# Kernel tuning notes

Measured on AMD Instinct MI355X. Metric: run time of the kernel, lower is better.

## Reference

```python
import jax, jax.numpy as jnp
import numpy as np
from jax import lax

B, C, H, W = 64, 384, 28, 28
E, K, R = 3, 2, 8          # num_experts, top_k, lora rank
HID = 4 * C                # ConvNeXt MLP hidden
EPS = 1e-6
SCALING = 8.0 / 8.0        # alpha / r


def setup_inputs() -> dict:
    key = jax.random.key(0)
    ks = jax.random.split(key, 18)
    N = B * H * W
    f32 = jnp.float32
    inp = {
        "x": jax.random.normal(ks[0], (B, C, H, W), f32),
        "conv_w": jax.random.normal(ks[1], (C, 1, 7, 7), f32) * 0.05,
        "conv_b": jax.random.normal(ks[2], (C,), f32) * 0.02,
        "norm_g": 1.0 + jax.random.normal(ks[3], (C,), f32) * 0.02,
        "norm_b": jax.random.normal(ks[4], (C,), f32) * 0.02,
        "dom_g": jax.random.normal(ks[5], (E, C), f32) * 0.02,
        "dom_b": jax.random.normal(ks[6], (E, C), f32) * 0.02,
        "fc1_w": jax.random.normal(ks[7], (C, HID), f32) * (C ** -0.5),
        "fc1_b": jax.random.normal(ks[8], (HID,), f32) * 0.02,
        "fc2_w": jax.random.normal(ks[9], (HID, C), f32) * (HID ** -0.5),
        "fc2_b": jax.random.normal(ks[10], (C,), f32) * 0.02,
        "w_down": jax.random.normal(ks[11], (E, C, R), f32) * (C ** -0.5),
        "w_up": jax.random.normal(ks[12], (E, R, C), f32) * 0.02,
        "gamma": jax.random.normal(ks[13], (C,), f32) * 0.1,
        "routing_weights": jax.nn.softmax(jax.random.normal(ks[14], (B, E), f32), axis=-1),
        "topk_probs": jax.nn.softmax(jax.random.normal(ks[15], (N, K), f32), axis=-1),
        "topk_indices": jax.random.randint(ks[16], (N, K), 0, E),
    }
    return inp


def _forward(x, conv_w, conv_b, norm_g, norm_b, dom_g, dom_b,
             fc1_w, fc1_b, fc2_w, fc2_b, w_down, w_up, gamma,
             routing_weights, topk_probs, topk_indices):
    shortcut = x
    # depthwise 7x7 conv, NCHW, SAME padding
    y = lax.conv_general_dilated(
        x, conv_w, window_strides=(1, 1), padding=((3, 3), (3, 3)),
        feature_group_count=C,
        dimension_numbers=("NCHW", "OIHW", "NCHW"))
    y = y + conv_b[None, :, None, None]
    y = jnp.transpose(y, (0, 2, 3, 1))  # [B, H, W, C] channels-last path

    # ParallelMoELayerNorm: orig LN + sum_i w_i * LN_i(x). All LNs share eps,
    # so normalize once and fuse affine params per-sample.
    mu = jnp.mean(y, axis=-1, keepdims=True)
    var = jnp.mean(jnp.square(y - mu), axis=-1, keepdims=True)
    xhat = (y - mu) * lax.rsqrt(var + EPS)
    g_eff = norm_g[None, :] + routing_weights @ dom_g   # [B, C]
    b_eff = norm_b[None, :] + routing_weights @ dom_b   # [B, C]
    y = xhat * g_eff[:, None, None, :] + b_eff[:, None, None, :]

    # base ConvNeXt MLP (exact GELU, as torch nn.GELU)
    h = jax.nn.gelu(jnp.einsum("bhwc,cf->bhwf", y, fc1_w) + fc1_b,
                    approximate=False)
    orig_out = jnp.einsum("bhwf,fc->bhwc", h, fc2_w) + fc2_b

    # MoE LoRA: dense per-expert rank-8 compute, combined with top-k weights.
    # Equivalent math to the gather/matmul/scatter-add loop in the source.
    y_flat = y.reshape(-1, C)                                   # [N, C]
    down = jnp.einsum("nc,ecr->enr", y_flat, w_down)            # [E, N, R]
    up = jnp.einsum("enr,erc->enc", jax.nn.gelu(down, approximate=False), w_up)
    # combine weights: comb[n, e] = sum_k topk_probs[n, k] * (topk_indices[n,k]==e)
    comb = jnp.sum(jax.nn.one_hot(topk_indices, E, dtype=y.dtype)
                   * topk_probs[..., None], axis=1)             # [N, E]
    moe_out = jnp.einsum("enc,ne->nc", up * SCALING, comb)
    y = orig_out + moe_out.reshape(B, H, W, C)

    y = jnp.transpose(y, (0, 3, 1, 2))  # back to NCHW
    y = gamma[None, :, None, None] * y  # layer scale; drop_path = identity (eval)
    return y + shortcut


def reference(x, conv_w, conv_b, norm_g, norm_b, dom_g, dom_b,
              fc1_w, fc1_b, fc2_w, fc2_b, w_down, w_up, gamma,
              routing_weights, topk_probs, topk_indices):
    return _forward(x, conv_w, conv_b, norm_g, norm_b, dom_g, dom_b,
                    fc1_w, fc1_b, fc2_w, fc2_b, w_down, w_up, gamma,
                    routing_weights, topk_probs, topk_indices)
```

## Files before the change

### kernel.cpp

```cpp
#include <hip/hip_runtime.h>
#include <hip/hip_bf16.h>
#include <cstdint>
#include <cstddef>

constexpr int cB   = 64;
constexpr int cC   = 384;
constexpr int cH   = 28;
constexpr int cW   = 28;
constexpr int cHID = 1536;
constexpr int cNTOK = cB * cH * cW;
constexpr int cKP   = cHID + 64;
constexpr int cCH   = 2;
constexpr int cMR   = cNTOK / cCH;

typedef __attribute__((ext_vector_type(8))) short bf16x8;
typedef __attribute__((ext_vector_type(4))) float f32x4;

__device__ __forceinline__ float gelu_f(float x) {
  float u = 1.5957691216057308f * x * (1.0f + 0.044715f * x * x);
  float e = __expf(-u);
  return x / (1.0f + e);
}

__device__ __forceinline__ float bf16_to_f(unsigned short s) {
  return __uint_as_float(((unsigned)s) << 16);
}
__device__ __forceinline__ unsigned short f_to_bf16(float v) {
  __hip_bfloat16 hb = __float2bfloat16(v);
  return *reinterpret_cast<unsigned short*>(&hb);
}

__device__ __forceinline__ void gload_lds16(const void* g, void* l) {
  __builtin_amdgcn_global_load_lds(
      (const __attribute__((address_space(1))) unsigned int*)g,
      (__attribute__((address_space(3))) unsigned int*)l, 16, 0, 0);
}

__device__ __forceinline__ int xcd_remap(int b, int nwg) {
  int qn = nwg >> 3, rm = nwg & 7;
  int xcd = b & 7, off = b >> 3;
  return (xcd < rm) ? xcd * (qn + 1) + off
                    : rm * (qn + 1) + (xcd - rm) * qn + off;
}

__global__ __launch_bounds__(256) void prep_eff(
    const float* __restrict__ ng, const float* __restrict__ nb,
    const float* __restrict__ dg, const float* __restrict__ db,
    const float* __restrict__ rw, float* __restrict__ geff, float* __restrict__ beff) {
  int i = blockIdx.x * 256 + threadIdx.x;
  if (i >= cB * cC) return;
  int b = i / cC, c = i - b * cC;
  float g = ng[c], bb = nb[c];
#pragma unroll
  for (int e = 0; e < 3; ++e) {
    float r = rw[b * 3 + e];
    g += r * dg[e * cC + c];
    bb += r * db[e * cC + c];
  }
  geff[i] = g;
  beff[i] = bb;
}

__global__ __launch_bounds__(256) void transpose_bf16(
    const float* __restrict__ w, __hip_bfloat16* __restrict__ wt, int R0, int C0) {
  __shared__ float t[64][65];
  int c0 = blockIdx.x * 64, r0 = blockIdx.y * 64;
  for (int i = threadIdx.x; i < 64 * 64; i += 256) {
    int r = i >> 6, c = i & 63;
    t[r][c] = w[(size_t)(r0 + r) * C0 + c0 + c];
  }
  __syncthreads();
  for (int i = threadIdx.x; i < 64 * 64; i += 256) {
    int c = i >> 6, r = i & 63;
    wt[(size_t)(c0 + c) * R0 + r0 + r] = __float2bfloat16(t[r][c]);
  }
}

__global__ __launch_bounds__(256) void build_fc2t(
    const float* __restrict__ fc2w, const float* __restrict__ wu,
    __hip_bfloat16* __restrict__ fc2t) {
  int i = blockIdx.x * 256 + threadIdx.x;
  if (i >= cC * cKP) return;
  int c = i / cKP, k = i - c * cKP;
  float v = 0.f;
  if (k < cHID) v = fc2w[(size_t)k * cC + c];
  else {
    int j = k - cHID;
    if (j < 24) v = wu[(size_t)(j >> 3) * 8 * cC + (size_t)(j & 7) * cC + c];
  }
  fc2t[i] = __float2bfloat16(v);
}

__global__ __launch_bounds__(256) void build_wdt(
    const float* __restrict__ wd, __hip_bfloat16* __restrict__ wdt) {
  int i = blockIdx.x * 256 + threadIdx.x;
  if (i >= 32 * cC) return;
  int j = i / cC, c = i - j * cC;
  float v = 0.f;
  if (j < 24) v = wd[(size_t)(j >> 3) * cC * 8 + (size_t)c * 8 + (j & 7)];
  wdt[i] = __float2bfloat16(v);
}

constexpr int cPL = 4;
__global__ __launch_bounds__(128) void conv_dw(
    const float* __restrict__ x, const float* __restrict__ cw,
    const float* __restrict__ cb, __hip_bfloat16* __restrict__ out) {
  int pb = blockIdx.x * cPL;
  int c0 = pb % cC;
  __shared__ __align__(16) float tile[cPL][34][38];
  __shared__ float wsm[cPL][49];
  const int tid = threadIdx.x;

  float2 z2 = {0.f, 0.f};
  for (int i = tid; i < cPL * 34 * 38 / 2; i += 128)
    ((float2*)tile)[i] = z2;
  __syncthreads();

  for (int i = tid; i < cPL * 196; i += 128) {
    int p = i / 196, q = i - p * 196;
    int r = q / 7, cl = (q - r * 7) * 4;
    float4 v = *(const float4*)&x[(size_t)(pb + p) * 784 + r * 28 + cl];
    float* dst = &tile[p][r + 3][cl + 4];
    *(float2*)dst = make_float2(v.x, v.y);
    *(float2*)(dst + 2) = make_float2(v.z, v.w);
  }
  for (int i = tid; i < cPL * 49; i += 128) {
    int p = i / 49, k = i - p * 49;
    wsm[p][k] = cw[(size_t)(c0 + p) * 49 + k];
  }
  __syncthreads();

  if (tid < cPL * 28) {
    int p = tid / 28, r = tid - p * 28;
    float acc[28];
    float cbv = cb[c0 + p];
#pragma unroll
    for (int w = 0; w < 28; ++w) acc[w] = cbv;
    for (int dh = 0; dh < 7; ++dh) {
      float rowv[36];
      const float* rp = &tile[p][r + dh][0];
#pragma unroll
      for (int k = 0; k < 18; ++k)
        ((float2*)rowv)[k] = *(const float2*)(rp + k * 2);
      float w7[7];
#pragma unroll
      for (int dw = 0; dw < 7; ++dw) w7[dw] = wsm[p][dh * 7 + dw];
#pragma unroll
      for (int w = 0; w < 28; ++w)
#pragma unroll
        for (int dw = 0; dw < 7; ++dw)
          acc[w] += rowv[w + dw + 1] * w7[dw];
    }
    unsigned short* op = (unsigned short*)out + (size_t)(pb + p) * 784 + r * 28;
#pragma unroll
    for (int k = 0; k < 7; ++k) {
      ushort4 s;
      s.x = f_to_bf16(acc[k * 4 + 0]);
      s.y = f_to_bf16(acc[k * 4 + 1]);
      s.z = f_to_bf16(acc[k * 4 + 2]);
      s.w = f_to_bf16(acc[k * 4 + 3]);
      *(ushort4*)&op[k * 4] = s;
    }
  }
}

__global__ __launch_bounds__(256) void ln_affine(
    const __hip_bfloat16* __restrict__ convout, const float* __restrict__ geff,
    const float* __restrict__ beff, __hip_bfloat16* __restrict__ y) {
  int bh = blockIdx.x;
  int b = bh / cH;
  int hrow = bh - b * cH;
  __shared__ float t[cC * 29];
  const unsigned short* src =
      (const unsigned short*)convout + (size_t)b * cC * (cH * cW) + (size_t)hrow * cW;
  for (int i = threadIdx.x; i < cC * 7; i += 256) {
    int c = i / 7, wq = (i - c * 7) * 4;
    ushort4 v = *(const ushort4*)&src[(size_t)c * (cH * cW) + wq];
    t[c * 29 + wq + 0] = bf16_to_f(v.x);
    t[c * 29 + wq + 1] = bf16_to_f(v.y);
    t[c * 29 + wq + 2] = bf16_to_f(v.z);
    t[c * 29 + wq + 3] = bf16_to_f(v.w);
  }
  __syncthreads();
  int wave = threadIdx.x >> 6, lane = threadIdx.x & 63;
  const float* gp = geff + (size_t)b * cC;
  const float* bp = beff + (size_t)b * cC;
  for (int w = wave; w < cW; w += 4) {
    float v[6], s = 0.f, s2 = 0.f;
#pragma unroll
    for (int j = 0; j < 6; ++j) {
      v[j] = t[(lane + 64 * j) * 29 + w];
      s += v[j];
      s2 += v[j] * v[j];
    }
#pragma unroll
    for (int d = 32; d; d >>= 1) {
      s += __shfl_xor(s, d);
      s2 += __shfl_xor(s2, d);
    }
    float mu = s * (1.0f / cC);
    float var = s2 * (1.0f / cC) - mu * mu;
    float rstd = rsqrtf(var + 1e-6f);
    size_t n = (size_t)bh * cW + w;
#pragma unroll
    for (int j = 0; j < 6; ++j) {
      int c = lane + 64 * j;
      float val = (v[j] - mu) * rstd * gp[c] + bp[c];
      y[n * cC + c] = __float2bfloat16(val);
    }
  }
}

template <int DO_GELU>
__global__ __launch_bounds__(512) void gemm8(
    const __hip_bfloat16* __restrict__ A, int lda,
    const __hip_bfloat16* __restrict__ Bt,
    const float* __restrict__ bias,
    __hip_bfloat16* __restrict__ Cb, int ldc,
    int M, int N, int K, int NT_N) {
  __shared__ __align__(16) __hip_bfloat16 As[3][256 * 64];
  __shared__ __align__(16) __hip_bfloat16 Bs[3][128 * 64];

  const int bid = xcd_remap(blockIdx.x, gridDim.x);
  const int gsz = 8 * NT_N;
  const int g = bid / gsz;
  const int q = bid - g * gsz;
  const int mi = g * 8 + q / NT_N;
  const int ni = q - (q / NT_N) * NT_N;
  const int m0 = mi * 256, n0 = ni * 128;

  const int tid = threadIdx.x;
  const int lane = tid & 63;
  const int wid = tid >> 6;
  const int wm = wid >> 1;
  const int wn = wid & 1;
  const int l15 = lane & 15, l7 = lane & 7, lq = lane >> 4;

  const __hip_bfloat16* srcA[4];
  const __hip_bfloat16* srcB[2];
  int dstA[4], dstB[2];
#pragma unroll
  for (int a = 0; a < 4; ++a) {
    int gu = a * 512 + tid;
    int row = gu >> 3, pu = gu & 7;
    int u = pu ^ (row & 7);
    srcA[a] = &A[(size_t)(m0 + row) * lda + u * 8];
    dstA[a] = gu * 16;
  }
#pragma unroll
  for (int b = 0; b < 2; ++b) {
    int gu = b * 512 + tid;
    int row = gu >> 3, pu = gu & 7;
    int u = pu ^ (row & 7);
    srcB[b] = &Bt[(size_t)(n0 + row) * K + u * 8];
    dstB[b] = gu * 16;
  }

#define STAGE_A(BUF)                                         \
  do {                                                       \
    _Pragma("unroll") for (int a = 0; a < 4; ++a) {          \
      gload_lds16(srcA[a], (char*)As[BUF] + dstA[a]);        \
      srcA[a] += 64;                                         \
    }                                                        \
  } while (0)
#define STAGE_B(BUF)                                         \
  do {                                                       \
    _Pragma("unroll") for (int b = 0; b < 2; ++b) {          \
      gload_lds16(srcB[b], (char*)Bs[BUF] + dstB[b]);        \
      srcB[b] += 64;                                         \
    }                                                        \
  } while (0)

  int roA[2][4], roB[2][4];
#pragma unroll
  for (int kh = 0; kh < 2; ++kh) {
    int pu = (kh * 4 + lq) ^ l7;
#pragma unroll
    for (int i = 0; i < 4; ++i) {
      roA[kh][i] = (wm * 64 + i * 16 + l15) * 128 + pu * 16;
      roB[kh][i] = (wn * 64 + i * 16 + l15) * 128 + pu * 16;
    }
  }

  const int nt = K >> 6;

  STAGE_A(0); STAGE_B(0);
  STAGE_A(1); STAGE_B(1);
  asm volatile("s_waitcnt vmcnt(6)" ::: "memory");
  __builtin_amdgcn_sched_barrier(0);
  __builtin_amdgcn_s_barrier();
  __builtin_amdgcn_sched_barrier(0);

  f32x4 acc[4][4] = {};
  int cur = 0, nx2 = 2;
  for (int t = 0; t < nt; ++t) {
    const char* asc = (const char*)As[cur];
    const char* bsc = (const char*)Bs[cur];

    bf16x8 a0[4], b0[4];
#pragma unroll
    for (int i = 0; i < 4; ++i) a0[i] = *(const bf16x8*)(asc + roA[0][i]);
#pragma unroll
    for (int j = 0; j < 4; ++j) b0[j] = *(const bf16x8*)(bsc + roB[0][j]);
    if (t + 2 < nt) STAGE_A(nx2);
    __builtin_amdgcn_s_setprio(1);
#pragma unroll
    for (int i = 0; i < 4; ++i)
#pragma unroll
      for (int j = 0; j < 4; ++j)
        acc[i][j] = __builtin_amdgcn_mfma_f32_16x16x32_bf16(a0[i], b0[j], acc[i][j], 0, 0, 0);
    __builtin_amdgcn_s_setprio(0);

    bf16x8 a1[4], b1[4];
#pragma unroll
    for (int i = 0; i < 4; ++i) a1[i] = *(const bf16x8*)(asc + roA[1][i]);
#pragma unroll
    for (int j = 0; j < 4; ++j) b1[j] = *(const bf16x8*)(bsc + roB[1][j]);
    if (t + 2 < nt) STAGE_B(nx2);
    __builtin_amdgcn_s_setprio(1);
#pragma unroll
    for (int i = 0; i < 4; ++i)
#pragma unroll
      for (int j = 0; j < 4; ++j)
        acc[i][j] = __builtin_amdgcn_mfma_f32_16x16x32_bf16(a1[i], b1[j], acc[i][j], 0, 0, 0);
    __builtin_amdgcn_s_setprio(0);

    if (t + 2 < nt) {
      asm volatile("s_waitcnt vmcnt(6)" ::: "memory");
    } else if (t + 1 < nt) {
      asm volatile("s_waitcnt vmcnt(0)" ::: "memory");
    }
    if (t + 1 < nt) {
      __builtin_amdgcn_sched_barrier(0);
      __builtin_amdgcn_s_barrier();
      __builtin_amdgcn_sched_barrier(0);
    }
    cur = (cur == 2) ? 0 : cur + 1;
    nx2 = (nx2 == 2) ? 0 : nx2 + 1;
  }
#undef STAGE_A
#undef STAGE_B

#pragma unroll
  for (int i = 0; i < 4; ++i) {
    int row = m0 + wm * 64 + i * 16 + (lane >> 4) * 4;
#pragma unroll
    for (int j = 0; j < 4; ++j) {
      int col = n0 + wn * 64 + j * 16 + (lane & 15);
      float bv = bias[col];
#pragma unroll
      for (int r = 0; r < 4; ++r) {
        float vv = acc[i][j][r] + bv;
        if (DO_GELU) vv = gelu_f(vv);
        Cb[(size_t)(row + r) * ldc + col] = __float2bfloat16(vv);
      }
    }
  }
}

__global__ __launch_bounds__(256) void lora_down(
    const __hip_bfloat16* __restrict__ y,
    const __hip_bfloat16* __restrict__ wdt,
    const float* __restrict__ probs,
    const int* __restrict__ inds,
    __hip_bfloat16* __restrict__ h) {
  __shared__ __align__(16) __hip_bfloat16 As[2][128 * 32];
  __shared__ __align__(16) __hip_bfloat16 Bsm[32 * 384];
  const int tid = threadIdx.x, lane = tid & 63, wid = tid >> 6;
  const int n0 = blockIdx.x * 128;

  for (int i = tid; i < 32 * 384 / 8; i += 256)
    ((bf16x8*)Bsm)[i] = ((const bf16x8*)wdt)[i];

  const int base0 = wid * 2048, base1 = base0 + 1024;
  const int off0 = base0 + lane * 16, off1 = base1 + lane * 16;
  const int row0 = off0 >> 6, col0 = (off0 >> 1) & 31;
  const int row1 = off1 >> 6, col1 = (off1 >> 1) & 31;
  const __hip_bfloat16* pa0 = &y[(size_t)(n0 + row0) * cC + col0];
  const __hip_bfloat16* pa1 = &y[(size_t)(n0 + row1) * cC + col1];

  const int nt = cC >> 5;
  gload_lds16(pa0, (char*)As[0] + base0);
  gload_lds16(pa1, (char*)As[0] + base1);
  pa0 += 32; pa1 += 32;
  __syncthreads();

  f32x4 acc[2][2] = {};
  int cur = 0;
  for (int t = 0; t < nt; ++t, cur ^= 1) {
    if (t + 1 < nt) {
      gload_lds16(pa0, (char*)As[cur ^ 1] + base0);
      gload_lds16(pa1, (char*)As[cur ^ 1] + base1);
      pa0 += 32; pa1 += 32;
    }
    int kt = t * 32;
    bf16x8 af[2], bfr[2];
#pragma unroll
    for (int i = 0; i < 2; ++i)
      af[i] = *(const bf16x8*)&As[cur][(wid * 32 + i * 16 + (lane & 15)) * 32 + (lane >> 4) * 8];
#pragma unroll
    for (int j = 0; j < 2; ++j)
      bfr[j] = *(const bf16x8*)&Bsm[(j * 16 + (lane & 15)) * 384 + kt + (lane >> 4) * 8];
#pragma unroll
    for (int i = 0; i < 2; ++i)
#pragma unroll
      for (int j = 0; j < 2; ++j)
        acc[i][j] = __builtin_amdgcn_mfma_f32_16x16x32_bf16(af[i], bfr[j], acc[i][j], 0, 0, 0);
    __syncthreads();
  }

#pragma unroll
  for (int i = 0; i < 2; ++i) {
#pragma unroll
    for (int j = 0; j < 2; ++j) {
      int colb = j * 16 + (lane & 15);
#pragma unroll
      for (int r = 0; r < 4; ++r) {
        int n = n0 + wid * 32 + i * 16 + (lane >> 4) * 4 + r;
        float zv = 0.f;
        if (colb < 24) {
          int e = colb >> 3;
          float comb = 0.f;
          if (inds[(size_t)n * 2] == e)     comb += probs[(size_t)n * 2];
          if (inds[(size_t)n * 2 + 1] == e) comb += probs[(size_t)n * 2 + 1];
          zv = comb * gelu_f(acc[i][j][r]);
        }
        h[(size_t)n * cKP + cHID + colb] = __float2bfloat16(zv);
        h[(size_t)n * cKP + cHID + 32 + colb] = __float2bfloat16(0.f);
      }
    }
  }
}

__global__ __launch_bounds__(256) void final_out(
    const __hip_bfloat16* __restrict__ tmp, const float* __restrict__ x,
    const float* __restrict__ gamma, float* __restrict__ out) {
  int bh = blockIdx.x;
  int b = bh / cH, hrow = bh - b * cH;
  __shared__ float t[cW * 385];
  const __hip_bfloat16* src = tmp + (size_t)bh * cW * cC;
  for (int i = threadIdx.x; i < cW * cC / 8; i += 256) {
    bf16x8 v = ((const bf16x8*)src)[i];
    int base = i * 8;
    int w = base / cC, c = base - w * cC;
#pragma unroll
    for (int k = 0; k < 8; ++k)
      t[w * 385 + c + k] = bf16_to_f((unsigned short)v[k]);
  }
  __syncthreads();
  const float* xb = x + (size_t)b * cC * (cH * cW) + (size_t)hrow * cW;
  float* ob = out + (size_t)b * cC * (cH * cW) + (size_t)hrow * cW;
  for (int i = threadIdx.x; i < cC * cW; i += 256) {
    int c = i / cW, w = i - c * cW;
    ob[(size_t)c * (cH * cW) + w] = gamma[c] * t[w * 385 + c] + xb[(size_t)c * (cH * cW) + w];
  }
}

extern "C" void kernel_launch(void* const* d_in, const int* in_sizes, int n_in,
                              void* d_out, int out_size, void* d_ws, size_t ws_size,
                              hipStream_t stream) {
  const float* x      = (const float*)d_in[0];
  const float* conv_w = (const float*)d_in[1];
  const float* conv_b = (const float*)d_in[2];
  const float* norm_g = (const float*)d_in[3];
  const float* norm_b = (const float*)d_in[4];
  const float* dom_g  = (const float*)d_in[5];
  const float* dom_b  = (const float*)d_in[6];
  const float* fc1_w  = (const float*)d_in[7];
  const float* fc1_b  = (const float*)d_in[8];
  const float* fc2_w  = (const float*)d_in[9];
  const float* fc2_b  = (const float*)d_in[10];
  const float* w_down = (const float*)d_in[11];
  const float* w_up   = (const float*)d_in[12];
  const float* gamma  = (const float*)d_in[13];
  const float* rw     = (const float*)d_in[14];
  const float* tkp    = (const float*)d_in[15];
  const int*   tki    = (const int*)d_in[16];
  float* out = (float*)d_out;

  char* ws = (char*)d_ws;
  __hip_bfloat16* y      = (__hip_bfloat16*)(ws + 0);
  __hip_bfloat16* tmpb   = (__hip_bfloat16*)(ws + 38535168);
  char*           hslot  = ws + 77070336;
  __hip_bfloat16* h      = (__hip_bfloat16*)hslot;
  __hip_bfloat16* convb  = (__hip_bfloat16*)hslot;
  __hip_bfloat16* fc1t   = (__hip_bfloat16*)(ws + 157351936);
  __hip_bfloat16* fc2t   = (__hip_bfloat16*)(ws + 158531584);
  __hip_bfloat16* wdt    = (__hip_bfloat16*)(ws + 159760384);
  float*          geff   = (float*)(ws + 159784960);
  float*          beff   = (float*)(ws + 159883264);

  prep_eff<<<(cB * cC + 255) / 256, 256, 0, stream>>>(norm_g, norm_b, dom_g, dom_b, rw, geff, beff);
  transpose_bf16<<<dim3(cHID / 64, cC / 64), 256, 0, stream>>>(fc1_w, fc1t, cC, cHID);
  build_fc2t<<<(cC * cKP + 255) / 256, 256, 0, stream>>>(fc2_w, w_up, fc2t);
  build_wdt<<<(32 * cC + 255) / 256, 256, 0, stream>>>(w_down, wdt);
  conv_dw<<<cB * cC / cPL, 128, 0, stream>>>(x, conv_w, conv_b, convb);
  ln_affine<<<cB * cH, 256, 0, stream>>>(convb, geff, beff, y);

  const int NTM8 = cMR / 256;
  for (int ch = 0; ch < cCH; ++ch) {
    const __hip_bfloat16* ych = y + (size_t)ch * cMR * cC;
    gemm8<1><<<NTM8 * (cHID / 128), 512, 0, stream>>>(
        ych, cC, fc1t, fc1_b, h, cKP, cMR, cHID, cC, cHID / 128);
    lora_down<<<cMR / 128, 256, 0, stream>>>(
        ych, wdt, tkp + (size_t)ch * cMR * 2, tki + (size_t)ch * cMR * 2, h);
    gemm8<0><<<NTM8 * (cC / 128), 512, 0, stream>>>(
        h, cKP, fc2t, fc2_b, tmpb + (size_t)ch * cMR * cC, cC, cMR, cC, cKP, cC / 128);
  }

  final_out<<<cB * cH, 256, 0, stream>>>(tmpb, x, gamma, out);
}
```

Baseline: 429.9 us.

## Use 4-wave GEMM with 128x64 per-wave tiles and interleaved prefetch

The 256x128 GEMM tile is now computed by 4 waves instead of 8, so each wave owns a 128x64 sub-tile with 32 accumulators. B fragments are reused across two A halves, which cuts LDS reads per MFMA. Global-to-LDS prefetches are spread over four MFMA phases. It drops the setprio hints and raises register pressure, and fewer waves per block means less latency hiding.

```diff
diff --git a/kernel.cpp b/kernel.cpp
--- a/kernel.cpp
+++ b/kernel.cpp
@@ -212,7 +212,7 @@
 }
 
 template <int DO_GELU>
-__global__ __launch_bounds__(512) void gemm8(
+__global__ __launch_bounds__(256) void gemm_p4(
     const __hip_bfloat16* __restrict__ A, int lda,
     const __hip_bfloat16* __restrict__ Bt,
     const float* __restrict__ bias,
@@ -236,97 +236,106 @@
   const int wn = wid & 1;
   const int l15 = lane & 15, l7 = lane & 7, lq = lane >> 4;
 
-  const __hip_bfloat16* srcA[4];
-  const __hip_bfloat16* srcB[2];
-  int dstA[4], dstB[2];
-#pragma unroll
-  for (int a = 0; a < 4; ++a) {
-    int gu = a * 512 + tid;
+  const __hip_bfloat16* srcA[8];
+  const __hip_bfloat16* srcB[4];
+  int dstA[8], dstB[4];
+#pragma unroll
+  for (int a = 0; a < 8; ++a) {
+    int gu = a * 256 + tid;
     int row = gu >> 3, pu = gu & 7;
     int u = pu ^ (row & 7);
     srcA[a] = &A[(size_t)(m0 + row) * lda + u * 8];
     dstA[a] = gu * 16;
   }
 #pragma unroll
-  for (int b = 0; b < 2; ++b) {
-    int gu = b * 512 + tid;
+  for (int b = 0; b < 4; ++b) {
+    int gu = b * 256 + tid;
     int row = gu >> 3, pu = gu & 7;
     int u = pu ^ (row & 7);
     srcB[b] = &Bt[(size_t)(n0 + row) * K + u * 8];
     dstB[b] = gu * 16;
   }
 
-#define STAGE_A(BUF)                                         \
-  do {                                                       \
-    _Pragma("unroll") for (int a = 0; a < 4; ++a) {          \
-      gload_lds16(srcA[a], (char*)As[BUF] + dstA[a]);        \
-      srcA[a] += 64;                                         \
-    }                                                        \
-  } while (0)
-#define STAGE_B(BUF)                                         \
-  do {                                                       \
-    _Pragma("unroll") for (int b = 0; b < 2; ++b) {          \
-      gload_lds16(srcB[b], (char*)Bs[BUF] + dstB[b]);        \
-      srcB[b] += 64;                                         \
-    }                                                        \
-  } while (0)
-
-  int roA[2][4], roB[2][4];
+#define SG_A(BUF, a) do { gload_lds16(srcA[a], (char*)As[BUF] + dstA[a]); srcA[a] += 64; } while (0)
+#define SG_B(BUF, b) do { gload_lds16(srcB[b], (char*)Bs[BUF] + dstB[b]); srcB[b] += 64; } while (0)
+
+  int roA[2][8], roB[2][4];
 #pragma unroll
   for (int kh = 0; kh < 2; ++kh) {
     int pu = (kh * 4 + lq) ^ l7;
 #pragma unroll
-    for (int i = 0; i < 4; ++i) {
-      roA[kh][i] = (wm * 64 + i * 16 + l15) * 128 + pu * 16;
-      roB[kh][i] = (wn * 64 + i * 16 + l15) * 128 + pu * 16;
-    }
+    for (int i = 0; i < 8; ++i)
+      roA[kh][i] = (wm * 128 + i * 16 + l15) * 128 + pu * 16;
+#pragma unroll
+    for (int j = 0; j < 4; ++j)
+      roB[kh][j] = (wn * 64 + j * 16 + l15) * 128 + pu * 16;
   }
 
   const int nt = K >> 6;
 
-  STAGE_A(0); STAGE_B(0);
-  STAGE_A(1); STAGE_B(1);
-  asm volatile("s_waitcnt vmcnt(6)" ::: "memory");
+#pragma unroll
+  for (int a = 0; a < 8; ++a) SG_A(0, a);
+#pragma unroll
+  for (int b = 0; b < 4; ++b) SG_B(0, b);
+#pragma unroll
+  for (int a = 0; a < 8; ++a) SG_A(1, a);
+#pragma unroll
+  for (int b = 0; b < 4; ++b) SG_B(1, b);
+  asm volatile("s_waitcnt vmcnt(12)" ::: "memory");
   __builtin_amdgcn_sched_barrier(0);
   __builtin_amdgcn_s_barrier();
   __builtin_amdgcn_sched_barrier(0);
 
-  f32x4 acc[4][4] = {};
+  f32x4 acc[8][4] = {};
   int cur = 0, nx2 = 2;
   for (int t = 0; t < nt; ++t) {
     const char* asc = (const char*)As[cur];
     const char* bsc = (const char*)Bs[cur];
-
-    bf16x8 a0[4], b0[4];
-#pragma unroll
-    for (int i = 0; i < 4; ++i) a0[i] = *(const bf16x8*)(asc + roA[0][i]);
-#pragma unroll
-    for (int j = 0; j < 4; ++j) b0[j] = *(const bf16x8*)(bsc + roB[0][j]);
-    if (t + 2 < nt) STAGE_A(nx2);
-    __builtin_amdgcn_s_setprio(1);
+    const bool pf = (t + 2 < nt);
+    bf16x8 aA[4], bb[4];
+
+#pragma unroll
+    for (int i = 0; i < 4; ++i) aA[i] = *(const bf16x8*)(asc + roA[0][i]);
+#pragma unroll
+    for (int j = 0; j < 4; ++j) bb[j] = *(const bf16x8*)(bsc + roB[0][j]);
+    if (pf) { SG_A(nx2, 0); SG_A(nx2, 1); SG_A(nx2, 2); }
 #pragma unroll
     for (int i = 0; i < 4; ++i)
 #pragma unroll
       for (int j = 0; j < 4; ++j)
-        acc[i][j] = __builtin_amdgcn_mfma_f32_16x16x32_bf16(a0[i], b0[j], acc[i][j], 0, 0, 0);
-    __builtin_amdgcn_s_setprio(0);
-
-    bf16x8 a1[4], b1[4];
-#pragma unroll
-    for (int i = 0; i < 4; ++i) a1[i] = *(const bf16x8*)(asc + roA[1][i]);
-#pragma unroll
-    for (int j = 0; j < 4; ++j) b1[j] = *(const bf16x8*)(bsc + roB[1][j]);
-    if (t + 2 < nt) STAGE_B(nx2);
-    __builtin_amdgcn_s_setprio(1);
+        acc[i][j] = __builtin_amdgcn_mfma_f32_16x16x32_bf16(aA[i], bb[j], acc[i][j], 0, 0, 0);
+
+#pragma unroll
+    for (int i = 0; i < 4; ++i) aA[i] = *(const bf16x8*)(asc + roA[0][i + 4]);
+    if (pf) { SG_A(nx2, 3); SG_A(nx2, 4); SG_A(nx2, 5); }
 #pragma unroll
     for (int i = 0; i < 4; ++i)
 #pragma unroll
       for (int j = 0; j < 4; ++j)
-        acc[i][j] = __builtin_amdgcn_mfma_f32_16x16x32_bf16(a1[i], b1[j], acc[i][j], 0, 0, 0);
-    __builtin_amdgcn_s_setprio(0);
-
-    if (t + 2 < nt) {
-      asm volatile("s_waitcnt vmcnt(6)" ::: "memory");
+        acc[i + 4][j] = __builtin_amdgcn_mfma_f32_16x16x32_bf16(aA[i], bb[j], acc[i + 4][j], 0, 0, 0);
+
+#pragma unroll
+    for (int i = 0; i < 4; ++i) aA[i] = *(const bf16x8*)(asc + roA[1][i]);
+#pragma unroll
+    for (int j = 0; j < 4; ++j) bb[j] = *(const bf16x8*)(bsc + roB[1][j]);
+    if (pf) { SG_A(nx2, 6); SG_A(nx2, 7); SG_B(nx2, 0); }
+#pragma unroll
+    for (int i = 0; i < 4; ++i)
+#pragma unroll
+      for (int j = 0; j < 4; ++j)
+        acc[i][j] = __builtin_amdgcn_mfma_f32_16x16x32_bf16(aA[i], bb[j], acc[i][j], 0, 0, 0);
+
+#pragma unroll
+    for (int i = 0; i < 4; ++i) aA[i] = *(const bf16x8*)(asc + roA[1][i + 4]);
+    if (pf) { SG_B(nx2, 1); SG_B(nx2, 2); SG_B(nx2, 3); }
+#pragma unroll
+    for (int i = 0; i < 4; ++i)
+#pragma unroll
+      for (int j = 0; j < 4; ++j)
+        acc[i + 4][j] = __builtin_amdgcn_mfma_f32_16x16x32_bf16(aA[i], bb[j], acc[i + 4][j], 0, 0, 0);
+
+    if (pf) {
+      asm volatile("s_waitcnt vmcnt(12)" ::: "memory");
     } else if (t + 1 < nt) {
       asm volatile("s_waitcnt vmcnt(0)" ::: "memory");
     }
@@ -338,15 +347,15 @@
     cur = (cur == 2) ? 0 : cur + 1;
     nx2 = (nx2 == 2) ? 0 : nx2 + 1;
   }
-#undef STAGE_A
-#undef STAGE_B
-
-#pragma unroll
-  for (int i = 0; i < 4; ++i) {
-    int row = m0 + wm * 64 + i * 16 + (lane >> 4) * 4;
+#undef SG_A
+#undef SG_B
+
+#pragma unroll
+  for (int i = 0; i < 8; ++i) {
+    int row = m0 + wm * 128 + i * 16 + lq * 4;
 #pragma unroll
     for (int j = 0; j < 4; ++j) {
-      int col = n0 + wn * 64 + j * 16 + (lane & 15);
+      int col = n0 + wn * 64 + j * 16 + l15;
       float bv = bias[col];
 #pragma unroll
       for (int r = 0; r < 4; ++r) {
@@ -497,14 +506,14 @@
   conv_dw<<<cB * cC / cPL, 128, 0, stream>>>(x, conv_w, conv_b, convb);
   ln_affine<<<cB * cH, 256, 0, stream>>>(convb, geff, beff, y);
 
-  const int NTM8 = cMR / 256;
+  const int NTM = cMR / 256;
   for (int ch = 0; ch < cCH; ++ch) {
     const __hip_bfloat16* ych = y + (size_t)ch * cMR * cC;
-    gemm8<1><<<NTM8 * (cHID / 128), 512, 0, stream>>>(
+    gemm_p4<1><<<NTM * (cHID / 128), 256, 0, stream>>>(
         ych, cC, fc1t, fc1_b, h, cKP, cMR, cHID, cC, cHID / 128);
     lora_down<<<cMR / 128, 256, 0, stream>>>(
         ych, wdt, tkp + (size_t)ch * cMR * 2, tki + (size_t)ch * cMR * 2, h);
-    gemm8<0><<<NTM8 * (cC / 128), 512, 0, stream>>>(
+    gemm_p4<0><<<NTM * (cC / 128), 256, 0, stream>>>(
         h, cKP, fc2t, fc2_b, tmpb + (size_t)ch * cMR * cC, cC, cMR, cC, cKP, cC / 128);
   }
 
```

Measured after the change: 566.3 us. 1.32x slower.

## Launch GEMMs over all tokens and re-schedule k-loop with finer barriers

Applied to the files above, without the earlier changes.

The fc1/lora/fc2 sequence now runs once over all tokens instead of in two chunks, so the hidden buffer grows and the workspace offsets of the weight buffers move. The GEMM main loop is restructured so the global-to-LDS prefetch is split evenly across the two k-halves, with extra workgroup barriers and lgkmcnt waits around each MFMA block. The single launch cuts launch count and tail effects. The added barriers may cost synchronization time and reduce overlap, and the larger workspace must fit the allocation.

```diff
diff --git a/kernel.cpp b/kernel.cpp
--- a/kernel.cpp
+++ b/kernel.cpp
@@ -10,8 +10,6 @@
 constexpr int cHID = 1536;
 constexpr int cNTOK = cB * cH * cW;
 constexpr int cKP   = cHID + 64;
-constexpr int cCH   = 2;
-constexpr int cMR   = cNTOK / cCH;
 
 typedef __attribute__((ext_vector_type(8))) short bf16x8;
 typedef __attribute__((ext_vector_type(4))) float f32x4;
@@ -256,20 +254,8 @@
     dstB[b] = gu * 16;
   }
 
-#define STAGE_A(BUF)                                         \
-  do {                                                       \
-    _Pragma("unroll") for (int a = 0; a < 4; ++a) {          \
-      gload_lds16(srcA[a], (char*)As[BUF] + dstA[a]);        \
-      srcA[a] += 64;                                         \
-    }                                                        \
-  } while (0)
-#define STAGE_B(BUF)                                         \
-  do {                                                       \
-    _Pragma("unroll") for (int b = 0; b < 2; ++b) {          \
-      gload_lds16(srcB[b], (char*)Bs[BUF] + dstB[b]);        \
-      srcB[b] += 64;                                         \
-    }                                                        \
-  } while (0)
+#define SG_A(BUF, a) do { gload_lds16(srcA[a], (char*)As[BUF] + dstA[a]); srcA[a] += 64; } while (0)
+#define SG_B(BUF, b) do { gload_lds16(srcB[b], (char*)Bs[BUF] + dstB[b]); srcB[b] += 64; } while (0)
 
   int roA[2][4], roB[2][4];
 #pragma unroll
@@ -284,8 +270,14 @@
 
   const int nt = K >> 6;
 
-  STAGE_A(0); STAGE_B(0);
-  STAGE_A(1); STAGE_B(1);
+#pragma unroll
+  for (int a = 0; a < 4; ++a) SG_A(0, a);
+#pragma unroll
+  for (int b = 0; b < 2; ++b) SG_B(0, b);
+#pragma unroll
+  for (int a = 0; a < 4; ++a) SG_A(1, a);
+#pragma unroll
+  for (int b = 0; b < 2; ++b) SG_B(1, b);
   asm volatile("s_waitcnt vmcnt(6)" ::: "memory");
   __builtin_amdgcn_sched_barrier(0);
   __builtin_amdgcn_s_barrier();
@@ -296,61 +288,70 @@
   for (int t = 0; t < nt; ++t) {
     const char* asc = (const char*)As[cur];
     const char* bsc = (const char*)Bs[cur];
-
-    bf16x8 a0[4], b0[4];
-#pragma unroll
-    for (int i = 0; i < 4; ++i) a0[i] = *(const bf16x8*)(asc + roA[0][i]);
-#pragma unroll
-    for (int j = 0; j < 4; ++j) b0[j] = *(const bf16x8*)(bsc + roB[0][j]);
-    if (t + 2 < nt) STAGE_A(nx2);
+    const bool pf = (t + 2 < nt);
+    bf16x8 av[4], bv[4];
+
+#pragma unroll
+    for (int i = 0; i < 4; ++i) av[i] = *(const bf16x8*)(asc + roA[0][i]);
+#pragma unroll
+    for (int j = 0; j < 4; ++j) bv[j] = *(const bf16x8*)(bsc + roB[0][j]);
+    if (pf) { SG_A(nx2, 0); SG_A(nx2, 1); SG_A(nx2, 2); }
+    __builtin_amdgcn_sched_barrier(0);
+    __builtin_amdgcn_s_barrier();
+    asm volatile("s_waitcnt lgkmcnt(0)" ::: "memory");
+    __builtin_amdgcn_sched_barrier(0);
     __builtin_amdgcn_s_setprio(1);
 #pragma unroll
     for (int i = 0; i < 4; ++i)
 #pragma unroll
       for (int j = 0; j < 4; ++j)
-        acc[i][j] = __builtin_amdgcn_mfma_f32_16x16x32_bf16(a0[i], b0[j], acc[i][j], 0, 0, 0);
+        acc[i][j] = __builtin_amdgcn_mfma_f32_16x16x32_bf16(av[i], bv[j], acc[i][j], 0, 0, 0);
     __builtin_amdgcn_s_setprio(0);
-
-    bf16x8 a1[4], b1[4];
-#pragma unroll
-    for (int i = 0; i < 4; ++i) a1[i] = *(const bf16x8*)(asc + roA[1][i]);
-#pragma unroll
-    for (int j = 0; j < 4; ++j) b1[j] = *(const bf16x8*)(bsc + roB[1][j]);
-    if (t + 2 < nt) STAGE_B(nx2);
-    __builtin_amdgcn_s_setprio(1);
-#pragma unroll
-    for (int i = 0; i < 4; ++i)
-#pragma unroll
-      for (int j = 0; j < 4; ++j)
-        acc[i][j] = __builtin_amdgcn_mfma_f32_16x16x32_bf16(a1[i], b1[j], acc[i][j], 0, 0, 0);
-    __builtin_amdgcn_s_setprio(0);
-
-    if (t + 2 < nt) {
+    __builtin_amdgcn_sched_barrier(0);
+    __builtin_amdgcn_s_barrier();
+    __builtin_amdgcn_sched_barrier(0);
+
+#pragma unroll
+    for (int i = 0; i < 4; ++i) av[i] = *(const bf16x8*)(asc + roA[1][i]);
+#pragma unroll
+    for (int j = 0; j < 4; ++j) bv[j] = *(const bf16x8*)(bsc + roB[1][j]);
+    if (pf) { SG_A(nx2, 3); SG_B(nx2, 0); SG_B(nx2, 1); }
+    if (pf) {
       asm volatile("s_waitcnt vmcnt(6)" ::: "memory");
     } else if (t + 1 < nt) {
       asm volatile("s_waitcnt vmcnt(0)" ::: "memory");
     }
-    if (t + 1 < nt) {
-      __builtin_amdgcn_sched_barrier(0);
-      __builtin_amdgcn_s_barrier();
-      __builtin_amdgcn_sched_barrier(0);
-    }
+    __builtin_amdgcn_sched_barrier(0);
+    __builtin_amdgcn_s_barrier();
+    asm volatile("s_waitcnt lgkmcnt(0)" ::: "memory");
+    __builtin_amdgcn_sched_barrier(0);
+    __builtin_amdgcn_s_setprio(1);
+#pragma unroll
+    for (int i = 0; i < 4; ++i)
+#pragma unroll
+      for (int j = 0; j < 4; ++j)
+        acc[i][j] = __builtin_amdgcn_mfma_f32_16x16x32_bf16(av[i], bv[j], acc[i][j], 0, 0, 0);
+    __builtin_amdgcn_s_setprio(0);
+    __builtin_amdgcn_sched_barrier(0);
+    __builtin_amdgcn_s_barrier();
+    __builtin_amdgcn_sched_barrier(0);
+
     cur = (cur == 2) ? 0 : cur + 1;
     nx2 = (nx2 == 2) ? 0 : nx2 + 1;
   }
-#undef STAGE_A
-#undef STAGE_B
+#undef SG_A
+#undef SG_B
 
 #pragma unroll
   for (int i = 0; i < 4; ++i) {
-    int row = m0 + wm * 64 + i * 16 + (lane >> 4) * 4;
+    int row = m0 + wm * 64 + i * 16 + lq * 4;
 #pragma unroll
     for (int j = 0; j < 4; ++j) {
-      int col = n0 + wn * 64 + j * 16 + (lane & 15);
-      float bv = bias[col];
+      int col = n0 + wn * 64 + j * 16 + l15;
+      float bv2 = bias[col];
 #pragma unroll
       for (int r = 0; r < 4; ++r) {
-        float vv = acc[i][j][r] + bv;
+        float vv = acc[i][j][r] + bv2;
         if (DO_GELU) vv = gelu_f(vv);
         Cb[(size_t)(row + r) * ldc + col] = __float2bfloat16(vv);
       }
@@ -484,11 +485,11 @@
   char*           hslot  = ws + 77070336;
   __hip_bfloat16* h      = (__hip_bfloat16*)hslot;
   __hip_bfloat16* convb  = (__hip_bfloat16*)hslot;
-  __hip_bfloat16* fc1t   = (__hip_bfloat16*)(ws + 157351936);
-  __hip_bfloat16* fc2t   = (__hip_bfloat16*)(ws + 158531584);
-  __hip_bfloat16* wdt    = (__hip_bfloat16*)(ws + 159760384);
-  float*          geff   = (float*)(ws + 159784960);
-  float*          beff   = (float*)(ws + 159883264);
+  __hip_bfloat16* fc1t   = (__hip_bfloat16*)(ws + 237633536);
+  __hip_bfloat16* fc2t   = (__hip_bfloat16*)(ws + 238813184);
+  __hip_bfloat16* wdt    = (__hip_bfloat16*)(ws + 240041984);
+  float*          geff   = (float*)(ws + 240066560);
+  float*          beff   = (float*)(ws + 240164864);
 
   prep_eff<<<(cB * cC + 255) / 256, 256, 0, stream>>>(norm_g, norm_b, dom_g, dom_b, rw, geff, beff);
   transpose_bf16<<<dim3(cHID / 64, cC / 64), 256, 0, stream>>>(fc1_w, fc1t, cC, cHID);
@@ -497,16 +498,12 @@
   conv_dw<<<cB * cC / cPL, 128, 0, stream>>>(x, conv_w, conv_b, convb);
   ln_affine<<<cB * cH, 256, 0, stream>>>(convb, geff, beff, y);
 
-  const int NTM8 = cMR / 256;
-  for (int ch = 0; ch < cCH; ++ch) {
-    const __hip_bfloat16* ych = y + (size_t)ch * cMR * cC;
-    gemm8<1><<<NTM8 * (cHID / 128), 512, 0, stream>>>(
-        ych, cC, fc1t, fc1_b, h, cKP, cMR, cHID, cC, cHID / 128);
-    lora_down<<<cMR / 128, 256, 0, stream>>>(
-        ych, wdt, tkp + (size_t)ch * cMR * 2, tki + (size_t)ch * cMR * 2, h);
-    gemm8<0><<<NTM8 * (cC / 128), 512, 0, stream>>>(
-        h, cKP, fc2t, fc2_b, tmpb + (size_t)ch * cMR * cC, cC, cMR, cC, cKP, cC / 128);
-  }
+  const int NTM = cNTOK / 256;
+  gemm8<1><<<NTM * (cHID / 128), 512, 0, stream>>>(
+      y, cC, fc1t, fc1_b, h, cKP, cNTOK, cHID, cC, cHID / 128);
+  lora_down<<<cNTOK / 128, 256, 0, stream>>>(y, wdt, tkp, tki, h);
+  gemm8<0><<<NTM * (cC / 128), 512, 0, stream>>>(
+      h, cKP, fc2t, fc2_b, tmpb, cC, cNTOK, cC, cKP, cC / 128);
 
   final_out<<<cB * cH, 256, 0, stream>>>(tmpb, x, gamma, out);
 }
```

Result: faster. 417.1 us (-3.0%).
